# Kernel optimization log

Hardware: AMD Instinct MI355X
Metric: run time of the kernel (lower is better)

Reference implementation:

```python
import jax, jax.numpy as jnp
import numpy as np

B, TE, TD, H = 8, 512, 256, 256  # batch, enc len, dec len, hidden (He==Hd)

def setup_inputs() -> dict:
    key = jax.random.key(0)
    k1, k2, k3, k4, k5 = jax.random.split(key, 5)
    # Keras 'uniform' initializer: U(-0.05, 0.05)
    u = lambda k, s: jax.random.uniform(k, s, jnp.float32, -0.05, 0.05)
    return {
        "encoder_out_seq": jax.random.normal(k1, (B, TE, H), jnp.float32),
        "decoder_out_seq": jax.random.normal(k2, (B, TD, H), jnp.float32),
        "W_a": u(k3, (H, H)),
        "U_a": u(k4, (H, H)),
        "V_a": u(k5, (H, 1)),
    }

def reference(encoder_out_seq, decoder_out_seq, W_a, U_a, V_a):
    # Bahdanau additive attention, fully batched (same math as the per-step K.rnn loop)
    We = jnp.einsum('bih,hk->bik', encoder_out_seq, W_a)   # [B,Te,H]
    Uh = jnp.einsum('bjh,hk->bjk', decoder_out_seq, U_a)   # [B,Td,H]
    # energies: V_a^T tanh(We_i + Uh_j)  -> [B,Td,Te]
    t = jnp.tanh(We[:, None, :, :] + Uh[:, :, None, :])    # [B,Td,Te,H]
    e = jnp.einsum('bjih,h->bji', t, V_a[:, 0])             # [B,Td,Te]
    e = jax.nn.softmax(e, axis=-1)                          # softmax over encoder positions
    c = jnp.einsum('bji,bih->bjh', e, encoder_out_seq)      # [B,Td,H]
    return (c, e)
```

## Files before the change

kernel.cpp:

```cpp
#include <hip/hip_runtime.h>


#define BB 8
#define TE 512
#define TD 256
#define HH 256

#define EXP2F(x) __builtin_amdgcn_exp2f(x)
#define RCPF(x)  __builtin_amdgcn_rcpf(x)
#define KSCALE   2.8853900817779268f
#define NSC      (-2.8853900817779268f)

typedef _Float16 h4 __attribute__((ext_vector_type(4)));
typedef _Float16 h8 __attribute__((ext_vector_type(8)));

__global__ __launch_bounds__(256) void k_pre(
    const float* __restrict__ enc, const float* __restrict__ dec,
    const float* __restrict__ Wa,  const float* __restrict__ Ua,
    _Float16* __restrict__ W4h, float* __restrict__ Uhe)
{
    const int tid = threadIdx.x;
    const bool is_enc = blockIdx.x < 256;
    const int bi = is_enc ? blockIdx.x : (blockIdx.x - 256);
    const int m0 = (bi >> 2) * 64;
    const int n0 = (bi & 3) * 64;
    const float* X = is_enc ? enc : dec;
    const float* W = is_enc ? Wa : Ua;

    __shared__ float Xs[32][68];
    __shared__ float Ws[32][68];

    const int kq = tid & 7,  xr = tid >> 3;
    const int wk = tid >> 3, wn = (tid & 7) * 8;
    const int tx = tid & 15, ty = tid >> 4;

    float acc[4][4];
    #pragma unroll
    for (int r = 0; r < 4; r++)
        #pragma unroll
        for (int c = 0; c < 4; c++) acc[r][c] = 0.f;

    for (int kc = 0; kc < HH; kc += 32) {
        float4 xa = *(const float4*)(X + (size_t)(m0 + xr) * HH + kc + kq * 4);
        float4 xb = *(const float4*)(X + (size_t)(m0 + xr + 32) * HH + kc + kq * 4);
        float4 wa = *(const float4*)(W + (size_t)(kc + wk) * HH + n0 + wn);
        float4 wb = *(const float4*)(W + (size_t)(kc + wk) * HH + n0 + wn + 4);
        __syncthreads();
        Xs[kq * 4 + 0][xr] = xa.x; Xs[kq * 4 + 1][xr] = xa.y;
        Xs[kq * 4 + 2][xr] = xa.z; Xs[kq * 4 + 3][xr] = xa.w;
        Xs[kq * 4 + 0][xr + 32] = xb.x; Xs[kq * 4 + 1][xr + 32] = xb.y;
        Xs[kq * 4 + 2][xr + 32] = xb.z; Xs[kq * 4 + 3][xr + 32] = xb.w;
        *(float4*)&Ws[wk][wn]     = wa;
        *(float4*)&Ws[wk][wn + 4] = wb;
        __syncthreads();
        #pragma unroll
        for (int k = 0; k < 32; k++) {
            float4 a = *(const float4*)&Xs[k][ty * 4];
            float4 b = *(const float4*)&Ws[k][tx * 4];
            acc[0][0] = fmaf(a.x, b.x, acc[0][0]); acc[0][1] = fmaf(a.x, b.y, acc[0][1]);
            acc[0][2] = fmaf(a.x, b.z, acc[0][2]); acc[0][3] = fmaf(a.x, b.w, acc[0][3]);
            acc[1][0] = fmaf(a.y, b.x, acc[1][0]); acc[1][1] = fmaf(a.y, b.y, acc[1][1]);
            acc[1][2] = fmaf(a.y, b.z, acc[1][2]); acc[1][3] = fmaf(a.y, b.w, acc[1][3]);
            acc[2][0] = fmaf(a.z, b.x, acc[2][0]); acc[2][1] = fmaf(a.z, b.y, acc[2][1]);
            acc[2][2] = fmaf(a.z, b.z, acc[2][2]); acc[2][3] = fmaf(a.z, b.w, acc[2][3]);
            acc[3][0] = fmaf(a.w, b.x, acc[3][0]); acc[3][1] = fmaf(a.w, b.y, acc[3][1]);
            acc[3][2] = fmaf(a.w, b.z, acc[3][2]); acc[3][3] = fmaf(a.w, b.w, acc[3][3]);
        }
    }

    if (is_enc) {
        const int b  = m0 >> 9;
        const int ib = (m0 & 511) + ty * 4;
        const int hh = n0 + tx * 4;
        const int o  = hh >> 3;
        const int hf = (hh & 7);
        #pragma unroll
        for (int r = 0; r < 4; r++) {
            h4 v;
            v.x = (_Float16)EXP2F(acc[r][0] * KSCALE);
            v.y = (_Float16)EXP2F(acc[r][1] * KSCALE);
            v.z = (_Float16)EXP2F(acc[r][2] * KSCALE);
            v.w = (_Float16)EXP2F(acc[r][3] * KSCALE);
            *(h4*)(W4h + (((size_t)b * 32 + o) * TE + ib + r) * 8 + hf) = v;
        }
    } else {
        #pragma unroll
        for (int r = 0; r < 4; r++) {
            float4 v;
            v.x = EXP2F(acc[r][0] * KSCALE); v.y = EXP2F(acc[r][1] * KSCALE);
            v.z = EXP2F(acc[r][2] * KSCALE); v.w = EXP2F(acc[r][3] * KSCALE);
            *(float4*)(Uhe + (size_t)(m0 + ty * 4 + r) * HH + n0 + tx * 4) = v;
        }
    }
}

__global__ __launch_bounds__(512, 4) void k_attn(
    const float* __restrict__ enc, const _Float16* __restrict__ W4h,
    const float* __restrict__ Uhe, const float* __restrict__ Va,
    float* __restrict__ out_c, float* __restrict__ out_e)
{
    const int wv = threadIdx.x >> 6, lane = threadIdx.x & 63;
    const int b   = blockIdx.x & 7;
    const int j0  = (blockIdx.x >> 3) * 4;
    const int jj0 = b * TD + j0;

    __shared__ float sP[4][TE];
    __shared__ float sR[8][4][HH];

    const int i = (wv << 6) + lane;
    const _Float16* wp = W4h + ((size_t)b * 32 * TE + i) * 8;
    const float* ua = Uhe + (size_t)jj0 * HH;
    const float* va = Va;

    float a0 = 0.f, a1 = 0.f, a2 = 0.f, a3 = 0.f;

#define OSTEP(ACC, UA, UB)                                                \
    {                                                                     \
        float A0 = fmaf(w0, (UA).x, 1.f);                                 \
        float A1 = fmaf(w1, (UA).y, 1.f);                                 \
        float A2 = fmaf(w2, (UA).z, 1.f);                                 \
        float A3 = fmaf(w3, (UA).w, 1.f);                                 \
        float A4 = fmaf(w4, (UB).x, 1.f);                                 \
        float A5 = fmaf(w5, (UB).y, 1.f);                                 \
        float A6 = fmaf(w6, (UB).z, 1.f);                                 \
        float A7 = fmaf(w7, (UB).w, 1.f);                                 \
        float dab = A0 * A1, dcd = A2 * A3;                               \
        float def_ = A4 * A5, dgh = A6 * A7;                              \
        float nab = fmaf(v4a.x, A1, v4a.y * A0);                          \
        float ncd = fmaf(v4a.z, A3, v4a.w * A2);                          \
        float nef = fmaf(v4b.x, A5, v4b.y * A4);                          \
        float ngh = fmaf(v4b.z, A7, v4b.w * A6);                          \
        float den4a = dab * dcd,  den4b = def_ * dgh;                     \
        float num4a = fmaf(nab, dcd, ncd * dab);                          \
        float num4b = fmaf(nef, dgh, ngh * def_);                         \
        float num = fmaf(num4a, den4b, num4b * den4a);                    \
        ACC = fmaf(num, RCPF(den4a * den4b), ACC);                        \
    }

    h8 w_pf[4];
    #pragma unroll
    for (int k = 0; k < 4; k++)
        w_pf[k] = *(const h8*)(wp + (size_t)k * TE * 8);

    #pragma unroll
    for (int q0 = 0; q0 < 32; q0 += 4) {
        h8 wg[4];
        #pragma unroll
        for (int k = 0; k < 4; k++) wg[k] = w_pf[k];
        #pragma unroll
        for (int k = 0; k < 4; k++) {
            int qq = q0 + 4 + k; if (qq > 31) qq = 31;
            w_pf[k] = *(const h8*)(wp + (size_t)qq * TE * 8);
        }
        #pragma unroll
        for (int k = 0; k < 4; k++) {
            const int q = q0 + k;
            float w0 = (float)wg[k][0], w1 = (float)wg[k][1];
            float w2 = (float)wg[k][2], w3 = (float)wg[k][3];
            float w4 = (float)wg[k][4], w5 = (float)wg[k][5];
            float w6 = (float)wg[k][6], w7 = (float)wg[k][7];
            float4 v4a = *(const float4*)(va + 8 * q);
            float4 v4b = *(const float4*)(va + 8 * q + 4);
            float4 u0a = *(const float4*)(ua + 8 * q);
            float4 u0b = *(const float4*)(ua + 8 * q + 4);
            float4 u1a = *(const float4*)(ua + HH + 8 * q);
            float4 u1b = *(const float4*)(ua + HH + 8 * q + 4);
            float4 u2a = *(const float4*)(ua + 2 * HH + 8 * q);
            float4 u2b = *(const float4*)(ua + 2 * HH + 8 * q + 4);
            float4 u3a = *(const float4*)(ua + 3 * HH + 8 * q);
            float4 u3b = *(const float4*)(ua + 3 * HH + 8 * q + 4);
            OSTEP(a0, u0a, u0b)
            OSTEP(a1, u1a, u1b)
            OSTEP(a2, u2a, u2b)
            OSTEP(a3, u3a, u3b)
        }
    }
#undef OSTEP

    sP[0][i] = NSC * a0;
    sP[1][i] = NSC * a1;
    sP[2][i] = NSC * a2;
    sP[3][i] = NSC * a3;
    __syncthreads();

    if (wv < 4) {
        float ev[8];
        float m = -3.0e38f;
        #pragma unroll
        for (int k = 0; k < 8; k++) {
            ev[k] = sP[wv][lane + 64 * k];
            m = fmaxf(m, ev[k]);
        }
        #pragma unroll
        for (int off = 32; off; off >>= 1) m = fmaxf(m, __shfl_xor(m, off, 64));
        float s = 0.f;
        #pragma unroll
        for (int k = 0; k < 8; k++) { ev[k] = EXP2F(ev[k] - m); s += ev[k]; }
        #pragma unroll
        for (int off = 32; off; off >>= 1) s += __shfl_xor(s, off, 64);
        float rs = RCPF(s);
        float* oe = out_e + (size_t)(jj0 + wv) * TE;
        #pragma unroll
        for (int k = 0; k < 8; k++) {
            float p = ev[k] * rs;
            sP[wv][lane + 64 * k] = p;
            oe[lane + 64 * k] = p;
        }
    }
    __syncthreads();

    const int ib = wv << 6;
    const float* eb = enc + ((size_t)b * TE + ib) * HH + 4 * lane;
    float4 c0 = {0,0,0,0}, c1 = {0,0,0,0}, c2 = {0,0,0,0}, c3 = {0,0,0,0};
    #pragma unroll 2
    for (int k4 = 0; k4 < 16; k4++) {
        float4 p0 = *(const float4*)&sP[0][ib + 4 * k4];
        float4 p1 = *(const float4*)&sP[1][ib + 4 * k4];
        float4 p2 = *(const float4*)&sP[2][ib + 4 * k4];
        float4 p3 = *(const float4*)&sP[3][ib + 4 * k4];
        const float* ep = eb + (size_t)k4 * 4 * HH;
        float4 q0 = *(const float4*)(ep);
        float4 q1 = *(const float4*)(ep + HH);
        float4 q2 = *(const float4*)(ep + 2 * HH);
        float4 q3 = *(const float4*)(ep + 3 * HH);
        c0.x = fmaf(p0.x, q0.x, c0.x); c0.y = fmaf(p0.x, q0.y, c0.y);
        c0.z = fmaf(p0.x, q0.z, c0.z); c0.w = fmaf(p0.x, q0.w, c0.w);
        c1.x = fmaf(p1.x, q0.x, c1.x); c1.y = fmaf(p1.x, q0.y, c1.y);
        c1.z = fmaf(p1.x, q0.z, c1.z); c1.w = fmaf(p1.x, q0.w, c1.w);
        c2.x = fmaf(p2.x, q0.x, c2.x); c2.y = fmaf(p2.x, q0.y, c2.y);
        c2.z = fmaf(p2.x, q0.z, c2.z); c2.w = fmaf(p2.x, q0.w, c2.w);
        c3.x = fmaf(p3.x, q0.x, c3.x); c3.y = fmaf(p3.x, q0.y, c3.y);
        c3.z = fmaf(p3.x, q0.z, c3.z); c3.w = fmaf(p3.x, q0.w, c3.w);
        c0.x = fmaf(p0.y, q1.x, c0.x); c0.y = fmaf(p0.y, q1.y, c0.y);
        c0.z = fmaf(p0.y, q1.z, c0.z); c0.w = fmaf(p0.y, q1.w, c0.w);
        c1.x = fmaf(p1.y, q1.x, c1.x); c1.y = fmaf(p1.y, q1.y, c1.y);
        c1.z = fmaf(p1.y, q1.z, c1.z); c1.w = fmaf(p1.y, q1.w, c1.w);
        c2.x = fmaf(p2.y, q1.x, c2.x); c2.y = fmaf(p2.y, q1.y, c2.y);
        c2.z = fmaf(p2.y, q1.z, c2.z); c2.w = fmaf(p2.y, q1.w, c2.w);
        c3.x = fmaf(p3.y, q1.x, c3.x); c3.y = fmaf(p3.y, q1.y, c3.y);
        c3.z = fmaf(p3.y, q1.z, c3.z); c3.w = fmaf(p3.y, q1.w, c3.w);
        c0.x = fmaf(p0.z, q2.x, c0.x); c0.y = fmaf(p0.z, q2.y, c0.y);
        c0.z = fmaf(p0.z, q2.z, c0.z); c0.w = fmaf(p0.z, q2.w, c0.w);
        c1.x = fmaf(p1.z, q2.x, c1.x); c1.y = fmaf(p1.z, q2.y, c1.y);
        c1.z = fmaf(p1.z, q2.z, c1.z); c1.w = fmaf(p1.z, q2.w, c1.w);
        c2.x = fmaf(p2.z, q2.x, c2.x); c2.y = fmaf(p2.z, q2.y, c2.y);
        c2.z = fmaf(p2.z, q2.z, c2.z); c2.w = fmaf(p2.z, q2.w, c2.w);
        c3.x = fmaf(p3.z, q2.x, c3.x); c3.y = fmaf(p3.z, q2.y, c3.y);
        c3.z = fmaf(p3.z, q2.z, c3.z); c3.w = fmaf(p3.z, q2.w, c3.w);
        c0.x = fmaf(p0.w, q3.x, c0.x); c0.y = fmaf(p0.w, q3.y, c0.y);
        c0.z = fmaf(p0.w, q3.z, c0.z); c0.w = fmaf(p0.w, q3.w, c0.w);
        c1.x = fmaf(p1.w, q3.x, c1.x); c1.y = fmaf(p1.w, q3.y, c1.y);
        c1.z = fmaf(p1.w, q3.z, c1.z); c1.w = fmaf(p1.w, q3.w, c1.w);
        c2.x = fmaf(p2.w, q3.x, c2.x); c2.y = fmaf(p2.w, q3.y, c2.y);
        c2.z = fmaf(p2.w, q3.z, c2.z); c2.w = fmaf(p2.w, q3.w, c2.w);
        c3.x = fmaf(p3.w, q3.x, c3.x); c3.y = fmaf(p3.w, q3.y, c3.y);
        c3.z = fmaf(p3.w, q3.z, c3.z); c3.w = fmaf(p3.w, q3.w, c3.w);
    }
    *(float4*)&sR[wv][0][4 * lane] = c0;
    *(float4*)&sR[wv][1][4 * lane] = c1;
    *(float4*)&sR[wv][2][4 * lane] = c2;
    *(float4*)&sR[wv][3][4 * lane] = c3;
    __syncthreads();

    {
        const int jr = wv & 3;
        const int h2 = (wv >> 2) * 128 + 2 * lane;
        float sx = 0.f, sy = 0.f;
        #pragma unroll
        for (int ww = 0; ww < 8; ww++) {
            float2 t = *(const float2*)&sR[ww][jr][h2];
            sx += t.x; sy += t.y;
        }
        float2 o; o.x = sx; o.y = sy;
        *(float2*)(out_c + (size_t)(jj0 + jr) * HH + h2) = o;
    }
}

extern "C" void kernel_launch(void* const* d_in, const int* in_sizes, int n_in,
                              void* d_out, int out_size, void* d_ws, size_t ws_size,
                              hipStream_t stream) {
    const float* enc = (const float*)d_in[0];
    const float* dec = (const float*)d_in[1];
    const float* Wa  = (const float*)d_in[2];
    const float* Ua  = (const float*)d_in[3];
    const float* Va  = (const float*)d_in[4];

    _Float16* W4h = (_Float16*)d_ws;
    float*    Uhe = (float*)(W4h + (size_t)BB * HH * TE);

    float* out_c = (float*)d_out;
    float* out_e = out_c + (size_t)BB * TD * HH;

    k_pre<<<384, 256, 0, stream>>>(enc, dec, Wa, Ua, W4h, Uhe);
    k_attn<<<BB * TD / 4, 512, 0, stream>>>(enc, W4h, Uhe, Va, out_c, out_e);
}
```

Measured before the change: 119.1 us.

## Store encoder exp projections in fp32 and drop manual prefetch pipeline

The encoder-side exp(2x) intermediate is now stored as fp32 in a float4-interleaved layout instead of fp16 packed in groups of 8. The attention inner loop becomes a simple unroll-by-2 loop that issues two float4 loads per step, replacing the explicit register prefetch pipeline. The occupancy hint in launch_bounds is also removed. This doubles intermediate memory traffic and register pressure in exchange for dropping fp16 conversions and simplifying the code, and fp32 may also improve accuracy.

```diff
diff --git a/kernel.cpp b/kernel.cpp
--- a/kernel.cpp
+++ b/kernel.cpp
@@ -11,13 +11,10 @@
 #define KSCALE   2.8853900817779268f
 #define NSC      (-2.8853900817779268f)
 
-typedef _Float16 h4 __attribute__((ext_vector_type(4)));
-typedef _Float16 h8 __attribute__((ext_vector_type(8)));
-
 __global__ __launch_bounds__(256) void k_pre(
     const float* __restrict__ enc, const float* __restrict__ dec,
     const float* __restrict__ Wa,  const float* __restrict__ Ua,
-    _Float16* __restrict__ W4h, float* __restrict__ Uhe)
+    float* __restrict__ W4, float* __restrict__ Uhe)
 {
     const int tid = threadIdx.x;
     const bool is_enc = blockIdx.x < 256;
@@ -71,17 +68,14 @@
     if (is_enc) {
         const int b  = m0 >> 9;
         const int ib = (m0 & 511) + ty * 4;
-        const int hh = n0 + tx * 4;
-        const int o  = hh >> 3;
-        const int hf = (hh & 7);
+        const int hq = (n0 >> 2) + tx;
+        float* dst = W4 + (((size_t)b * 64 + hq) * TE + ib) * 4;
         #pragma unroll
         for (int r = 0; r < 4; r++) {
-            h4 v;
-            v.x = (_Float16)EXP2F(acc[r][0] * KSCALE);
-            v.y = (_Float16)EXP2F(acc[r][1] * KSCALE);
-            v.z = (_Float16)EXP2F(acc[r][2] * KSCALE);
-            v.w = (_Float16)EXP2F(acc[r][3] * KSCALE);
-            *(h4*)(W4h + (((size_t)b * 32 + o) * TE + ib + r) * 8 + hf) = v;
+            float4 v;
+            v.x = EXP2F(acc[r][0] * KSCALE); v.y = EXP2F(acc[r][1] * KSCALE);
+            v.z = EXP2F(acc[r][2] * KSCALE); v.w = EXP2F(acc[r][3] * KSCALE);
+            *(float4*)(dst + (size_t)r * 4) = v;
         }
     } else {
         #pragma unroll
@@ -94,8 +88,8 @@
     }
 }
 
-__global__ __launch_bounds__(512, 4) void k_attn(
-    const float* __restrict__ enc, const _Float16* __restrict__ W4h,
+__global__ __launch_bounds__(512) void k_attn(
+    const float* __restrict__ enc, const float* __restrict__ W4,
     const float* __restrict__ Uhe, const float* __restrict__ Va,
     float* __restrict__ out_c, float* __restrict__ out_e)
 {
@@ -108,7 +102,7 @@
     __shared__ float sR[8][4][HH];
 
     const int i = (wv << 6) + lane;
-    const _Float16* wp = W4h + ((size_t)b * 32 * TE + i) * 8;
+    const float* wp = W4 + ((size_t)b * 64 * TE + i) * 4;
     const float* ua = Uhe + (size_t)jj0 * HH;
     const float* va = Va;
 
@@ -116,14 +110,14 @@
 
 #define OSTEP(ACC, UA, UB)                                                \
     {                                                                     \
-        float A0 = fmaf(w0, (UA).x, 1.f);                                 \
-        float A1 = fmaf(w1, (UA).y, 1.f);                                 \
-        float A2 = fmaf(w2, (UA).z, 1.f);                                 \
-        float A3 = fmaf(w3, (UA).w, 1.f);                                 \
-        float A4 = fmaf(w4, (UB).x, 1.f);                                 \
-        float A5 = fmaf(w5, (UB).y, 1.f);                                 \
-        float A6 = fmaf(w6, (UB).z, 1.f);                                 \
-        float A7 = fmaf(w7, (UB).w, 1.f);                                 \
+        float A0 = fmaf(wa.x, (UA).x, 1.f);                               \
+        float A1 = fmaf(wa.y, (UA).y, 1.f);                               \
+        float A2 = fmaf(wa.z, (UA).z, 1.f);                               \
+        float A3 = fmaf(wa.w, (UA).w, 1.f);                               \
+        float A4 = fmaf(wb.x, (UB).x, 1.f);                               \
+        float A5 = fmaf(wb.y, (UB).y, 1.f);                               \
+        float A6 = fmaf(wb.z, (UB).z, 1.f);                               \
+        float A7 = fmaf(wb.w, (UB).w, 1.f);                               \
         float dab = A0 * A1, dcd = A2 * A3;                               \
         float def_ = A4 * A5, dgh = A6 * A7;                              \
         float nab = fmaf(v4a.x, A1, v4a.y * A0);                          \
@@ -137,43 +131,24 @@
         ACC = fmaf(num, RCPF(den4a * den4b), ACC);                        \
     }
 
-    h8 w_pf[4];
-    #pragma unroll
-    for (int k = 0; k < 4; k++)
-        w_pf[k] = *(const h8*)(wp + (size_t)k * TE * 8);
-
-    #pragma unroll
-    for (int q0 = 0; q0 < 32; q0 += 4) {
-        h8 wg[4];
-        #pragma unroll
-        for (int k = 0; k < 4; k++) wg[k] = w_pf[k];
-        #pragma unroll
-        for (int k = 0; k < 4; k++) {
-            int qq = q0 + 4 + k; if (qq > 31) qq = 31;
-            w_pf[k] = *(const h8*)(wp + (size_t)qq * TE * 8);
-        }
-        #pragma unroll
-        for (int k = 0; k < 4; k++) {
-            const int q = q0 + k;
-            float w0 = (float)wg[k][0], w1 = (float)wg[k][1];
-            float w2 = (float)wg[k][2], w3 = (float)wg[k][3];
-            float w4 = (float)wg[k][4], w5 = (float)wg[k][5];
-            float w6 = (float)wg[k][6], w7 = (float)wg[k][7];
-            float4 v4a = *(const float4*)(va + 8 * q);
-            float4 v4b = *(const float4*)(va + 8 * q + 4);
-            float4 u0a = *(const float4*)(ua + 8 * q);
-            float4 u0b = *(const float4*)(ua + 8 * q + 4);
-            float4 u1a = *(const float4*)(ua + HH + 8 * q);
-            float4 u1b = *(const float4*)(ua + HH + 8 * q + 4);
-            float4 u2a = *(const float4*)(ua + 2 * HH + 8 * q);
-            float4 u2b = *(const float4*)(ua + 2 * HH + 8 * q + 4);
-            float4 u3a = *(const float4*)(ua + 3 * HH + 8 * q);
-            float4 u3b = *(const float4*)(ua + 3 * HH + 8 * q + 4);
-            OSTEP(a0, u0a, u0b)
-            OSTEP(a1, u1a, u1b)
-            OSTEP(a2, u2a, u2b)
-            OSTEP(a3, u3a, u3b)
-        }
+    #pragma unroll 2
+    for (int q = 0; q < 32; q++) {
+        float4 wa = *(const float4*)(wp + (size_t)(2 * q) * TE * 4);
+        float4 wb = *(const float4*)(wp + (size_t)(2 * q + 1) * TE * 4);
+        float4 v4a = *(const float4*)(va + 8 * q);
+        float4 v4b = *(const float4*)(va + 8 * q + 4);
+        float4 u0a = *(const float4*)(ua + 8 * q);
+        float4 u0b = *(const float4*)(ua + 8 * q + 4);
+        float4 u1a = *(const float4*)(ua + HH + 8 * q);
+        float4 u1b = *(const float4*)(ua + HH + 8 * q + 4);
+        float4 u2a = *(const float4*)(ua + 2 * HH + 8 * q);
+        float4 u2b = *(const float4*)(ua + 2 * HH + 8 * q + 4);
+        float4 u3a = *(const float4*)(ua + 3 * HH + 8 * q);
+        float4 u3b = *(const float4*)(ua + 3 * HH + 8 * q + 4);
+        OSTEP(a0, u0a, u0b)
+        OSTEP(a1, u1a, u1b)
+        OSTEP(a2, u2a, u2b)
+        OSTEP(a3, u3a, u3b)
     }
 #undef OSTEP
 
@@ -285,12 +260,12 @@
     const float* Ua  = (const float*)d_in[3];
     const float* Va  = (const float*)d_in[4];
 
-    _Float16* W4h = (_Float16*)d_ws;
-    float*    Uhe = (float*)(W4h + (size_t)BB * HH * TE);
+    float* W4  = (float*)d_ws;
+    float* Uhe = W4 + (size_t)BB * HH * TE;
 
     float* out_c = (float*)d_out;
     float* out_e = out_c + (size_t)BB * TD * HH;
 
-    k_pre<<<384, 256, 0, stream>>>(enc, dec, Wa, Ua, W4h, Uhe);
-    k_attn<<<BB * TD / 4, 512, 0, stream>>>(enc, W4h, Uhe, Va, out_c, out_e);
+    k_pre<<<384, 256, 0, stream>>>(enc, dec, Wa, Ua, W4, Uhe);
+    k_attn<<<BB * TD / 4, 512, 0, stream>>>(enc, W4, Uhe, Va, out_c, out_e);
 }
```

Result: faster. 114.2 us (-4.1%).
